# Kernel tuning notes

Hardware: AMD Instinct MI355X
Metric: run time of the kernel (lower is better)

## Reference

```python
import jax, jax.numpy as jnp
import numpy as np

B, T, C = 2, 2048, 2048
H, D, G = 16, 128, 4   # num_heads, head_dim, num_kv_groups
EPS = 1e-6


def setup_inputs() -> dict:
    key = jax.random.key(0)
    ks = jax.random.split(key, 6)
    x = jax.random.normal(ks[0], (B, T, C), dtype=jnp.float32)
    # causal mask: True = disallowed (strictly upper triangular)
    mask = jnp.triu(jnp.ones((T, T), dtype=bool), k=1)
    # RoPE tables, full head_dim with duplicated angle halves
    inv_freq = 1.0 / (10000.0 ** (jnp.arange(0, D, 2, dtype=jnp.float32) / D))
    angles = jnp.arange(T, dtype=jnp.float32)[:, None] * inv_freq[None, :]  # [T, D/2]
    angles = jnp.concatenate([angles, angles], axis=-1)                     # [T, D]
    cos, sin = jnp.cos(angles), jnp.sin(angles)
    std = 0.02
    W_query = jax.random.normal(ks[1], (C, H * D), dtype=jnp.float32) * std
    W_key = jax.random.normal(ks[2], (C, G * D), dtype=jnp.float32) * std
    W_value = jax.random.normal(ks[3], (C, G * D), dtype=jnp.float32) * std
    W_out = jax.random.normal(ks[4], (H * D, C), dtype=jnp.float32) * std
    q_scale = jnp.ones((D,), dtype=jnp.float32)
    k_scale = jnp.ones((D,), dtype=jnp.float32)
    return {"x": x, "mask": mask, "cos": cos, "sin": sin,
            "W_query": W_query, "W_key": W_key, "W_value": W_value,
            "W_out": W_out, "q_scale": q_scale, "k_scale": k_scale}


def _rmsnorm(x, scale):
    # qwen3-compatible: compute in fp32, rescale, cast back
    xf = x.astype(jnp.float32)
    var = jnp.mean(xf * xf, axis=-1, keepdims=True)
    return (xf * jax.lax.rsqrt(var + EPS) * scale).astype(x.dtype)


def _rope(x, cos, sin):
    d = x.shape[-1]
    x1, x2 = x[..., : d // 2], x[..., d // 2 :]
    rotated = jnp.concatenate([-x2, x1], axis=-1)
    # cos/sin: [T, D] -> broadcast over [B, H, T, D]
    return (x * cos[None, None] + rotated * sin[None, None]).astype(x.dtype)


def reference(x, mask, cos, sin, W_query, W_key, W_value, W_out, q_scale, k_scale):
    b, t, _ = x.shape
    Q = (x @ W_query).reshape(b, t, H, D).transpose(0, 2, 1, 3)  # [B,H,T,D]
    K = (x @ W_key).reshape(b, t, G, D).transpose(0, 2, 1, 3)    # [B,G,T,D]
    V = (x @ W_value).reshape(b, t, G, D).transpose(0, 2, 1, 3)
    group_size = H // G
    K = jnp.repeat(K, group_size, axis=1)  # [B,H,T,D]
    V = jnp.repeat(V, group_size, axis=1)
    Q = _rmsnorm(Q, q_scale)
    K = _rmsnorm(K, k_scale)
    Q = _rope(Q, cos, sin)
    K = _rope(K, cos, sin)
    scale = D ** (-0.5)
    attn = jnp.einsum("bhqd,bhkd->bhqk", Q, K) * scale
    attn = jnp.where(mask[None, None], -jnp.inf, attn)
    w = jax.nn.softmax(attn, axis=-1)
    out = jnp.einsum("bhqk,bhkd->bhqd", w, V)
    out = out.transpose(0, 2, 1, 3).reshape(b, t, H * D)
    return out @ W_out
```

## Files before the change

kernel.cpp:

```cpp
#include <hip/hip_runtime.h>
#include <hip/hip_bf16.h>

#define Bq 2
#define Tt 2048
#define Cc 2048
#define Hh 16
#define Dd 128
#define Gg 4

using bf16 = __hip_bfloat16;
typedef __attribute__((ext_vector_type(8))) short short8;
typedef __attribute__((ext_vector_type(4))) float f32x4;

__device__ __forceinline__ void gload_lds16(const void* g, void* l) {
    __builtin_amdgcn_global_load_lds(
        (const __attribute__((address_space(1))) unsigned int*)g,
        (__attribute__((address_space(3))) unsigned int*)l, 16, 0, 0);
}

#define MEMBAR() asm volatile("" ::: "memory")

__global__ void k_cast_bf16(const float* __restrict__ in, bf16* __restrict__ out, int n4) {
    int i = blockIdx.x * blockDim.x + threadIdx.x;
    if (i >= n4) return;
    float4 v = ((const float4*)in)[i];
    union { bf16 h[4]; uint2 u; } u;
    u.h[0] = __float2bfloat16(v.x);
    u.h[1] = __float2bfloat16(v.y);
    u.h[2] = __float2bfloat16(v.z);
    u.h[3] = __float2bfloat16(v.w);
    ((uint2*)out)[i] = u.u;
}

__global__ void k_cast_transpose(const float* __restrict__ in, bf16* __restrict__ out,
                                 int rows, int cols, int ostride) {
    __shared__ float tile[32][33];
    int c0 = blockIdx.x * 32, r0 = blockIdx.y * 32;
    int tx = threadIdx.x, ty = threadIdx.y;
    #pragma unroll
    for (int k = 0; k < 4; ++k)
        tile[ty + 8*k][tx] = in[(size_t)(r0 + ty + 8*k) * cols + c0 + tx];
    __syncthreads();
    #pragma unroll
    for (int k = 0; k < 4; ++k)
        out[(size_t)(c0 + ty + 8*k) * ostride + r0 + tx] = __float2bfloat16(tile[tx][ty + 8*k]);
}

__global__ void k_vt(const bf16* __restrict__ QKV, bf16* __restrict__ Vt) {
    __shared__ bf16 tile[64][65];
    const int d0 = blockIdx.x * 64, t0 = blockIdx.y * 64;
    const int bg = blockIdx.z;
    const int b = bg >> 2, g = bg & 3;
    const int tx = threadIdx.x, ty = threadIdx.y;
    const bf16* src = QKV + (size_t)(b * Tt) * 3072 + 2560 + g * 128;
    #pragma unroll
    for (int k = 0; k < 8; ++k)
        tile[ty + 8*k][tx] = src[(size_t)(t0 + ty + 8*k) * 3072 + d0 + tx];
    __syncthreads();
    bf16* dst = Vt + (size_t)bg * Dd * Tt;
    #pragma unroll
    for (int k = 0; k < 8; ++k)
        dst[(size_t)(d0 + ty + 8*k) * Tt + t0 + tx] = tile[tx][ty + 8*k];
}

template<int OUTF32>
__global__ __launch_bounds__(512, 2)
void k_gemm256(const bf16* __restrict__ A, const bf16* __restrict__ Bt,
               void* __restrict__ C, int M, int N, int K, int nbx) {
    __shared__ __align__(16) bf16 Ls[2][4][128 * 64];
    const int tid = threadIdx.x;
    const int lane = tid & 63;
    const int wid = tid >> 6;
    const int wm = wid >> 2, wn = wid & 3;

    const int nb = gridDim.x;
    const int cpx = nb >> 3;
    const int id = blockIdx.x;
    const int sid = (id & 7) * cpx + (id >> 3);
    const int bx = sid % nbx, by = sid / nbx;
    const int row0 = by * 256, col0 = bx * 256;

    const int NT = K >> 6;
    f32x4 acc[2][4][2][2] = {};

#define STAGE_HT(bufq, tt, ht) {                                               \
        const bool isB_ = ((ht) == 1 || (ht) == 2);                            \
        const int half_ = ((ht) >= 2) ? 128 : 0;                               \
        _Pragma("unroll")                                                      \
        for (int c_ = 0; c_ < 2; ++c_) {                                       \
            const int r_ = c_ * 64 + (tid >> 3);                               \
            const int ch_ = (tid & 7) ^ (r_ & 7);                              \
            const bf16* gs_ = (isB_ ? Bt + (size_t)(col0 + half_ + r_) * K     \
                                    : A  + (size_t)(row0 + half_ + r_) * K)    \
                              + (tt) * 64 + ch_ * 8;                           \
            gload_lds16(gs_, &Ls[bufq][ht][c_ * 4096] + tid * 8);              \
        } }

    STAGE_HT(0, 0, 0); STAGE_HT(0, 0, 1); STAGE_HT(0, 0, 2); STAGE_HT(0, 0, 3);

    for (int t = 0; t < NT; ++t) {
        const int p = t & 1, q = p ^ 1;
        const bool pf = (t + 1 < NT);
        const bf16* hA0 = Ls[p][0];
        const bf16* hB0 = Ls[p][1];
        const bf16* hB1 = Ls[p][2];
        const bf16* hA1 = Ls[p][3];

        short8 af[4][2], bb0[2][2], bb1[2][2];

        auto rdA = [&](const bf16* hh, int i, int kk) -> short8 {
            const int ra = wm * 64 + i * 16 + (lane & 15);
            return *(const short8*)((const char*)hh + ra * 128 +
                   ((kk * 64 + (lane >> 4) * 16) ^ ((ra & 7) << 4)));
        };
        auto rdB = [&](const bf16* hh, int j, int kk) -> short8 {
            const int rb = wn * 32 + j * 16 + (lane & 15);
            return *(const short8*)((const char*)hh + rb * 128 +
                   ((kk * 64 + (lane >> 4) * 16) ^ ((rb & 7) << 4)));
        };

        if (pf) { STAGE_HT(q, t + 1, 0); asm volatile("s_waitcnt vmcnt(6)" ::: "memory"); }
        else    { asm volatile("s_waitcnt vmcnt(4)" ::: "memory"); }
        __builtin_amdgcn_s_barrier(); MEMBAR();
        #pragma unroll
        for (int i = 0; i < 4; ++i)
            #pragma unroll
            for (int kk = 0; kk < 2; ++kk) af[i][kk] = rdA(hA0, i, kk);
        #pragma unroll
        for (int j = 0; j < 2; ++j)
            #pragma unroll
            for (int kk = 0; kk < 2; ++kk) bb0[j][kk] = rdB(hB0, j, kk);
        __builtin_amdgcn_s_setprio(1);
        #pragma unroll
        for (int i = 0; i < 4; ++i)
            #pragma unroll
            for (int j = 0; j < 2; ++j)
                #pragma unroll
                for (int kk = 0; kk < 2; ++kk)
                    acc[0][i][0][j] = __builtin_amdgcn_mfma_f32_16x16x32_bf16(af[i][kk], bb0[j][kk], acc[0][i][0][j], 0, 0, 0);
        __builtin_amdgcn_s_setprio(0);

        MEMBAR();
        if (pf) { STAGE_HT(q, t + 1, 1); asm volatile("s_waitcnt vmcnt(6)" ::: "memory"); }
        else    { asm volatile("s_waitcnt vmcnt(2)" ::: "memory"); }
        __builtin_amdgcn_s_barrier(); MEMBAR();
        #pragma unroll
        for (int j = 0; j < 2; ++j)
            #pragma unroll
            for (int kk = 0; kk < 2; ++kk) bb1[j][kk] = rdB(hB1, j, kk);
        __builtin_amdgcn_s_setprio(1);
        #pragma unroll
        for (int i = 0; i < 4; ++i)
            #pragma unroll
            for (int j = 0; j < 2; ++j)
                #pragma unroll
                for (int kk = 0; kk < 2; ++kk)
                    acc[0][i][1][j] = __builtin_amdgcn_mfma_f32_16x16x32_bf16(af[i][kk], bb1[j][kk], acc[0][i][1][j], 0, 0, 0);
        __builtin_amdgcn_s_setprio(0);

        MEMBAR();
        if (pf) { STAGE_HT(q, t + 1, 2); asm volatile("s_waitcnt vmcnt(6)" ::: "memory"); }
        else    { asm volatile("s_waitcnt vmcnt(0)" ::: "memory"); }
        __builtin_amdgcn_s_barrier(); MEMBAR();
        #pragma unroll
        for (int i = 0; i < 4; ++i)
            #pragma unroll
            for (int kk = 0; kk < 2; ++kk) af[i][kk] = rdA(hA1, i, kk);
        __builtin_amdgcn_s_setprio(1);
        #pragma unroll
        for (int i = 0; i < 4; ++i)
            #pragma unroll
            for (int j = 0; j < 2; ++j)
                #pragma unroll
                for (int kk = 0; kk < 2; ++kk)
                    acc[1][i][1][j] = __builtin_amdgcn_mfma_f32_16x16x32_bf16(af[i][kk], bb1[j][kk], acc[1][i][1][j], 0, 0, 0);
        __builtin_amdgcn_s_setprio(0);

        MEMBAR();
        if (pf) STAGE_HT(q, t + 1, 3);
        __builtin_amdgcn_s_setprio(1);
        #pragma unroll
        for (int i = 0; i < 4; ++i)
            #pragma unroll
            for (int j = 0; j < 2; ++j)
                #pragma unroll
                for (int kk = 0; kk < 2; ++kk)
                    acc[1][i][0][j] = __builtin_amdgcn_mfma_f32_16x16x32_bf16(af[i][kk], bb0[j][kk], acc[1][i][0][j], 0, 0, 0);
        __builtin_amdgcn_s_setprio(0);
        MEMBAR();
        __builtin_amdgcn_s_barrier();
        MEMBAR();
    }
#undef STAGE_HT

    #pragma unroll
    for (int mh = 0; mh < 2; ++mh)
        #pragma unroll
        for (int i = 0; i < 4; ++i)
            #pragma unroll
            for (int nh = 0; nh < 2; ++nh)
                #pragma unroll
                for (int j = 0; j < 2; ++j)
                    #pragma unroll
                    for (int r = 0; r < 4; ++r) {
                        const int crow = row0 + mh * 128 + wm * 64 + i * 16 + (lane >> 4) * 4 + r;
                        const int ccol = col0 + nh * 128 + wn * 32 + j * 16 + (lane & 15);
                        const size_t idx = (size_t)crow * N + ccol;
                        const float v = acc[mh][i][nh][j][r];
                        if (OUTF32) ((float*)C)[idx] = v;
                        else        ((bf16*)C)[idx] = __float2bfloat16(v);
                    }
}

template<int OUTF32>
__global__ __launch_bounds__(256)
void k_gemm_bt(const bf16* __restrict__ A, const bf16* __restrict__ Bt,
               void* __restrict__ C, int M, int N, int K) {
    __shared__ __align__(16) bf16 As[128 * 64];
    __shared__ __align__(16) bf16 Bs[128 * 64];
    const int lane = threadIdx.x & 63;
    const int wave = threadIdx.x >> 6;
    const int row0 = blockIdx.y * 128;
    const int col0 = blockIdx.x * 128;
    const int wm = wave >> 1, wn = wave & 1;
    f32x4 acc[4][4] = {};

    const int srow = lane >> 3;
    const int schunk = ((lane & 7) ^ srow) * 8;

    for (int k0 = 0; k0 < K; k0 += 64) {
        #pragma unroll
        for (int j = 0; j < 4; ++j) {
            const int c = j * 4 + wave;
            const int rt = c * 8 + srow;
            gload_lds16(A  + (size_t)(row0 + rt) * K + k0 + schunk, As + c * 512);
            gload_lds16(Bt + (size_t)(col0 + rt) * K + k0 + schunk, Bs + c * 512);
        }
        __syncthreads();
        #pragma unroll
        for (int kk = 0; kk < 2; ++kk) {
            short8 af[4], bfr[4];
            #pragma unroll
            for (int i = 0; i < 4; ++i) {
                const int ra = wm * 64 + i * 16 + (lane & 15);
                af[i] = *(const short8*)((const char*)As + ra * 128 +
                        ((kk * 64 + (lane >> 4) * 16) ^ ((ra & 7) << 4)));
                const int rb = wn * 64 + i * 16 + (lane & 15);
                bfr[i] = *(const short8*)((const char*)Bs + rb * 128 +
                        ((kk * 64 + (lane >> 4) * 16) ^ ((rb & 7) << 4)));
            }
            __builtin_amdgcn_s_setprio(1);
            #pragma unroll
            for (int i = 0; i < 4; ++i)
                #pragma unroll
                for (int j = 0; j < 4; ++j)
                    acc[i][j] = __builtin_amdgcn_mfma_f32_16x16x32_bf16(af[i], bfr[j], acc[i][j], 0, 0, 0);
            __builtin_amdgcn_s_setprio(0);
        }
        __syncthreads();
    }

    const int crow0 = row0 + wm * 64 + (lane >> 4) * 4;
    const int ccol0 = col0 + wn * 64 + (lane & 15);
    #pragma unroll
    for (int i = 0; i < 4; ++i)
        #pragma unroll
        for (int j = 0; j < 4; ++j)
            #pragma unroll
            for (int r = 0; r < 4; ++r) {
                const size_t idx = (size_t)(crow0 + i * 16 + r) * N + ccol0 + j * 16;
                const float v = acc[i][j][r];
                if (OUTF32) ((float*)C)[idx] = v;
                else        ((bf16*)C)[idx] = __float2bfloat16(v);
            }
}

__global__ void k_qkv_post(const bf16* __restrict__ QKV,
                           const float* __restrict__ cosT, const float* __restrict__ sinT,
                           const float* __restrict__ qs, const float* __restrict__ ks,
                           bf16* __restrict__ Qr, bf16* __restrict__ Kr) {
    const int bt = blockIdx.x;
    const int b = bt >> 11;
    const int t = bt & 2047;
    const int lane = threadIdx.x & 63;
    const int wave = threadIdx.x >> 6;
    const float c1 = cosT[t * 128 + lane],      c2 = cosT[t * 128 + 64 + lane];
    const float s1 = sinT[t * 128 + lane],      s2 = sinT[t * 128 + 64 + lane];
    const float qs1 = qs[lane], qs2 = qs[lane + 64];
    const float ks1 = ks[lane], ks2 = ks[lane + 64];
    const bf16* rowb = QKV + (size_t)bt * 3072;
    for (int rr = wave; rr < 20; rr += 4) {
        const bf16* src = rowb + rr * 128;
        const float x1 = __bfloat162float(src[lane]);
        const float x2 = __bfloat162float(src[lane + 64]);
        bf16* dst;
        if (rr < 16) dst = Qr + ((size_t)(b * Hh + rr) * Tt + t) * 128;
        else         dst = Kr + ((size_t)(b * Gg + (rr - 16)) * Tt + t) * 128;
        float ssum = x1 * x1 + x2 * x2;
        #pragma unroll
        for (int o = 32; o > 0; o >>= 1) ssum += __shfl_xor(ssum, o);
        const float inv = rsqrtf(ssum * (1.0f / 128.0f) + 1e-6f);
        const float post = (rr < 16) ? 0.08838834764831845f : 1.0f;
        const float sc1 = ((rr < 16) ? qs1 : ks1) * inv;
        const float sc2 = ((rr < 16) ? qs2 : ks2) * inv;
        const float y1 = x1 * sc1;
        const float y2 = x2 * sc2;
        dst[lane]      = __float2bfloat16((y1 * c1 - y2 * s1) * post);
        dst[lane + 64] = __float2bfloat16((y2 * c2 + y1 * s2) * post);
    }
}

__global__ __launch_bounds__(256)
void k_attn(const bf16* __restrict__ Qr, const bf16* __restrict__ Kr,
            const bf16* __restrict__ Vt, bf16* __restrict__ AO) {
    __shared__ __align__(16) bf16 Ksm[2][64 * 128];
    __shared__ __align__(16) bf16 Vsm[2][128 * 64];
    __shared__ __align__(16) bf16 Psm[4][16 * 64];
    const int id = blockIdx.x;
    const int bg = id & 7;
    const int wid = id >> 3;
    const int pair = wid & 15;
    const int hg = wid >> 4;
    const int b = bg >> 2, g = bg & 3;
    const int h = g * 4 + hg;
    const int lane = threadIdx.x & 63;
    const int wave = threadIdx.x >> 6;

    const bf16* Kbase = Kr + (size_t)(b * Gg + g) * Tt * Dd;
    const bf16* Vbase = Vt + (size_t)(b * Gg + g) * Dd * Tt;

    for (int pass = 0; pass < 2; ++pass) {
        const int qt = pass ? (31 - pair) : pair;
        const bf16* Qbase = Qr + ((size_t)(b * Hh + h) * Tt + qt * 64) * Dd;

        short8 qf[4];
        #pragma unroll
        for (int kk = 0; kk < 4; ++kk)
            qf[kk] = *(const short8*)(Qbase + (size_t)(wave * 16 + (lane & 15)) * 128 + kk * 32 + (lane >> 4) * 8);

        float l_run[4] = {0.f, 0.f, 0.f, 0.f};
        f32x4 oacc[8];
        #pragma unroll
        for (int j = 0; j < 8; ++j) oacc[j] = (f32x4){0.f, 0.f, 0.f, 0.f};

        {
            #pragma unroll
            for (int j = 0; j < 4; ++j) {
                const int c = j * 4 + wave;
                const int rtk = c * 4 + (lane >> 4);
                const int chk = (lane & 15) ^ (rtk & 7);
                gload_lds16(Kbase + (size_t)rtk * 128 + chk * 8, Ksm[0] + c * 512);
                const int rtv = c * 8 + (lane >> 3);
                const int chv = (lane & 7) ^ ((lane >> 3) & 7);
                gload_lds16(Vbase + (size_t)rtv * Tt + chv * 8, Vsm[0] + c * 512);
            }
        }

        int cur = 0;
        const int nkv = qt + 1;
        for (int tk = 0; tk < nkv; ++tk) {
            __syncthreads();

            if (tk + 1 < nkv) {
                const int k0n = (tk + 1) * 64;
                #pragma unroll
                for (int j = 0; j < 4; ++j) {
                    const int c = j * 4 + wave;
                    const int rtk = c * 4 + (lane >> 4);
                    const int chk = (lane & 15) ^ (rtk & 7);
                    gload_lds16(Kbase + (size_t)(k0n + rtk) * 128 + chk * 8, Ksm[cur ^ 1] + c * 512);
                    const int rtv = c * 8 + (lane >> 3);
                    const int chv = (lane & 7) ^ ((lane >> 3) & 7);
                    gload_lds16(Vbase + (size_t)rtv * Tt + k0n + chv * 8, Vsm[cur ^ 1] + c * 512);
                }
            }

            const bf16* Ks = Ksm[cur];
            const bf16* Vs = Vsm[cur];

            f32x4 s[4];
            #pragma unroll
            for (int nt = 0; nt < 4; ++nt) s[nt] = (f32x4){0.f, 0.f, 0.f, 0.f};
            __builtin_amdgcn_s_setprio(1);
            #pragma unroll
            for (int nt = 0; nt < 4; ++nt) {
                #pragma unroll
                for (int kk = 0; kk < 4; ++kk) {
                    const int rk = nt * 16 + (lane & 15);
                    short8 kf = *(const short8*)((const char*)Ks + rk * 256 +
                                ((kk * 64 + (lane >> 4) * 16) ^ ((rk & 7) << 4)));
                    s[nt] = __builtin_amdgcn_mfma_f32_16x16x32_bf16(qf[kk], kf, s[nt], 0, 0, 0);
                }
            }
            __builtin_amdgcn_s_setprio(0);

            if (tk == nkv - 1) {
                const int qrow = qt * 64 + wave * 16 + (lane >> 4) * 4;
                const int k0 = tk * 64;
                #pragma unroll
                for (int nt = 0; nt < 4; ++nt) {
                    const int kcol = k0 + nt * 16 + (lane & 15);
                    #pragma unroll
                    for (int r = 0; r < 4; ++r)
                        if (kcol > qrow + r) s[nt][r] = -1e30f;
                }
            }

            #pragma unroll
            for (int nt = 0; nt < 4; ++nt)
                #pragma unroll
                for (int r = 0; r < 4; ++r) {
                    const float p = __expf(s[nt][r]);
                    l_run[r] += p;
                    s[nt][r] = p;
                }

            #pragma unroll
            for (int nt = 0; nt < 4; ++nt)
                #pragma unroll
                for (int r = 0; r < 4; ++r) {
                    const int prow = (lane >> 4) * 4 + r;
                    const int pcol = nt * 16 + (lane & 15);
                    *(bf16*)((char*)Psm[wave] + ((prow * 128 + pcol * 2) ^ ((prow & 7) << 4))) =
                        __float2bfloat16(s[nt][r]);
                }
            #pragma unroll
            for (int kk = 0; kk < 2; ++kk) {
                const int pr = lane & 15;
                short8 pf = *(const short8*)((const char*)Psm[wave] + pr * 128 +
                            ((kk * 64 + (lane >> 4) * 16) ^ ((pr & 7) << 4)));
                __builtin_amdgcn_s_setprio(1);
                #pragma unroll
                for (int j = 0; j < 8; ++j) {
                    const int rb = j * 16 + (lane & 15);
                    short8 vf = *(const short8*)((const char*)Vs + rb * 128 +
                                ((kk * 64 + (lane >> 4) * 16) ^ ((rb & 7) << 4)));
                    oacc[j] = __builtin_amdgcn_mfma_f32_16x16x32_bf16(pf, vf, oacc[j], 0, 0, 0);
                }
                __builtin_amdgcn_s_setprio(0);
            }
            cur ^= 1;
        }
        __syncthreads();

        #pragma unroll
        for (int o = 1; o < 16; o <<= 1)
            #pragma unroll
            for (int r = 0; r < 4; ++r) l_run[r] += __shfl_xor(l_run[r], o);

        #pragma unroll
        for (int r = 0; r < 4; ++r) {
            const float inv = 1.0f / l_run[r];
            const int qrow = qt * 64 + wave * 16 + (lane >> 4) * 4 + r;
            bf16* dst = AO + (size_t)(b * Tt + qrow) * 2048 + h * 128 + (lane & 15);
            #pragma unroll
            for (int j = 0; j < 8; ++j)
                dst[j * 16] = __float2bfloat16(oacc[j][r] * inv);
        }
    }
}

extern "C" void kernel_launch(void* const* d_in, const int* in_sizes, int n_in,
                              void* d_out, int out_size, void* d_ws, size_t ws_size,
                              hipStream_t stream) {
    const float* x    = (const float*)d_in[0];
    const float* cosT = (const float*)d_in[2];
    const float* sinT = (const float*)d_in[3];
    const float* Wq   = (const float*)d_in[4];
    const float* Wk   = (const float*)d_in[5];
    const float* Wv   = (const float*)d_in[6];
    const float* Wo   = (const float*)d_in[7];
    const float* qs   = (const float*)d_in[8];
    const float* ks   = (const float*)d_in[9];

    char* ws = (char*)d_ws;
    bf16* xb   = (bf16*)(ws);
    bf16* Wcat = (bf16*)(ws + 16777216);
    bf16* Wot  = (bf16*)(ws + 29360128);
    bf16* QKV  = (bf16*)(ws + 37748736);
    bf16* Qr   = (bf16*)(ws + 62914560);
    bf16* Kr   = (bf16*)(ws + 79691776);
    bf16* Vtp  = (bf16*)(ws + 83886080);
    bf16* AO   = (bf16*)(ws + 88080384);

    k_cast_bf16<<<8192, 256, 0, stream>>>(x, xb, 2097152);
    dim3 tb(32, 8);
    k_cast_transpose<<<dim3(64, 64), tb, 0, stream>>>(Wq, Wcat, 2048, 2048, 2048);
    k_cast_transpose<<<dim3(16, 64), tb, 0, stream>>>(Wk, Wcat + (size_t)2048 * 2048, 2048, 512, 2048);
    k_cast_transpose<<<dim3(16, 64), tb, 0, stream>>>(Wv, Wcat + (size_t)2560 * 2048, 2048, 512, 2048);
    k_cast_transpose<<<dim3(64, 64), tb, 0, stream>>>(Wo, Wot, 2048, 2048, 2048);

    k_gemm256<0><<<192, 512, 0, stream>>>(xb, Wcat, QKV, 4096, 3072, 2048, 12);
    k_qkv_post<<<4096, 256, 0, stream>>>(QKV, cosT, sinT, qs, ks, Qr, Kr);
    k_vt<<<dim3(2, 32, 8), dim3(64, 8), 0, stream>>>(QKV, Vtp);
    k_attn<<<512, 256, 0, stream>>>(Qr, Kr, Vtp, AO);
    k_gemm_bt<1><<<dim3(16, 32), 256, 0, stream>>>(AO, Wot, d_out, 4096, 2048, 2048);
}
```

Before: 199.7 us.

## Split attention KV loop across two blocks by parity and merge partials

New measurement: 224.9 us. +12.6%, slower.

```diff
diff --git a/kernel.cpp b/kernel.cpp
--- a/kernel.cpp
+++ b/kernel.cpp
@@ -311,153 +311,206 @@
 }
 
 __global__ __launch_bounds__(256)
-void k_attn(const bf16* __restrict__ Qr, const bf16* __restrict__ Kr,
-            const bf16* __restrict__ Vt, bf16* __restrict__ AO) {
-    __shared__ __align__(16) bf16 Ksm[2][64 * 128];
-    __shared__ __align__(16) bf16 Vsm[2][128 * 64];
-    __shared__ __align__(16) bf16 Psm[4][16 * 64];
+void k_attn_part(const bf16* __restrict__ Qr, const bf16* __restrict__ Kr,
+                 const bf16* __restrict__ Vt,
+                 bf16* __restrict__ O0, bf16* __restrict__ O1,
+                 float* __restrict__ L0, float* __restrict__ L1) {
+    __shared__ __align__(16) bf16 Ksm[64 * 128];
+    __shared__ __align__(16) bf16 Vsm[128 * 64];
+    __shared__ __align__(16) bf16 Psm[4][32 * 64];
     const int id = blockIdx.x;
     const int bg = id & 7;
-    const int wid = id >> 3;
-    const int pair = wid & 15;
-    const int hg = wid >> 4;
+    const int rr = id >> 3;
+    const int par = rr & 1;
+    const int pairI = (rr >> 1) & 7;
+    const int hg = rr >> 4;
     const int b = bg >> 2, g = bg & 3;
     const int h = g * 4 + hg;
     const int lane = threadIdx.x & 63;
-    const int wave = threadIdx.x >> 6;
+    const int w = threadIdx.x >> 6;
+    const int hi = lane >> 4;
+    const int lq = lane & 15;
+
+    bf16* Op  = par ? O1 : O0;
+    float* Lp = par ? L1 : L0;
 
     const bf16* Kbase = Kr + (size_t)(b * Gg + g) * Tt * Dd;
     const bf16* Vbase = Vt + (size_t)(b * Gg + g) * Dd * Tt;
 
+#define STAGE_KV(k0_) {                                                        \
+        _Pragma("unroll")                                                      \
+        for (int j = 0; j < 4; ++j) {                                          \
+            const int c = j * 4 + w;                                           \
+            const int rtk = c * 4 + (lane >> 4);                               \
+            const int chk = (lane & 15) ^ (rtk & 7);                           \
+            gload_lds16(Kbase + (size_t)((k0_) + rtk) * 128 + chk * 8, Ksm + c * 512); \
+            const int rtv = c * 8 + (lane >> 3);                               \
+            const int chv = (lane & 7) ^ ((lane >> 3) & 7);                    \
+            gload_lds16(Vbase + (size_t)rtv * Tt + (k0_) + chv * 8, Vsm + c * 512);    \
+        } }
+
     for (int pass = 0; pass < 2; ++pass) {
-        const int qt = pass ? (31 - pair) : pair;
-        const bf16* Qbase = Qr + ((size_t)(b * Hh + h) * Tt + qt * 64) * Dd;
-
-        short8 qf[4];
-        #pragma unroll
-        for (int kk = 0; kk < 4; ++kk)
-            qf[kk] = *(const short8*)(Qbase + (size_t)(wave * 16 + (lane & 15)) * 128 + kk * 32 + (lane >> 4) * 8);
-
-        float l_run[4] = {0.f, 0.f, 0.f, 0.f};
-        f32x4 oacc[8];
-        #pragma unroll
-        for (int j = 0; j < 8; ++j) oacc[j] = (f32x4){0.f, 0.f, 0.f, 0.f};
-
-        {
-            #pragma unroll
-            for (int j = 0; j < 4; ++j) {
-                const int c = j * 4 + wave;
-                const int rtk = c * 4 + (lane >> 4);
-                const int chk = (lane & 15) ^ (rtk & 7);
-                gload_lds16(Kbase + (size_t)rtk * 128 + chk * 8, Ksm[0] + c * 512);
-                const int rtv = c * 8 + (lane >> 3);
-                const int chv = (lane & 7) ^ ((lane >> 3) & 7);
-                gload_lds16(Vbase + (size_t)rtv * Tt + chv * 8, Vsm[0] + c * 512);
-            }
-        }
-
-        int cur = 0;
-        const int nkv = qt + 1;
-        for (int tk = 0; tk < nkv; ++tk) {
+        const int qt = pass ? (15 - pairI) : pairI;
+        const int niter = qt + 1;
+        const bf16* Qbase = Qr + ((size_t)(b * Hh + h) * Tt + qt * 128) * Dd;
+
+        short8 qf[2][4];
+        #pragma unroll
+        for (int sub = 0; sub < 2; ++sub)
+            #pragma unroll
+            for (int kk = 0; kk < 4; ++kk)
+                qf[sub][kk] = *(const short8*)(Qbase +
+                    (size_t)(w * 32 + sub * 16 + lq) * 128 + kk * 32 + hi * 8);
+
+        float l_run[2][4] = {};
+        f32x4 oacc[2][8];
+        #pragma unroll
+        for (int sub = 0; sub < 2; ++sub)
+            #pragma unroll
+            for (int j = 0; j < 8; ++j) oacc[sub][j] = (f32x4){0.f, 0.f, 0.f, 0.f};
+
+        STAGE_KV(par * 64);
+
+        for (int i = 0; i < niter; ++i) {
+            const int tk = par + 2 * i;
             __syncthreads();
 
-            if (tk + 1 < nkv) {
-                const int k0n = (tk + 1) * 64;
-                #pragma unroll
-                for (int j = 0; j < 4; ++j) {
-                    const int c = j * 4 + wave;
-                    const int rtk = c * 4 + (lane >> 4);
-                    const int chk = (lane & 15) ^ (rtk & 7);
-                    gload_lds16(Kbase + (size_t)(k0n + rtk) * 128 + chk * 8, Ksm[cur ^ 1] + c * 512);
-                    const int rtv = c * 8 + (lane >> 3);
-                    const int chv = (lane & 7) ^ ((lane >> 3) & 7);
-                    gload_lds16(Vbase + (size_t)rtv * Tt + k0n + chv * 8, Vsm[cur ^ 1] + c * 512);
+            const bf16* Ks = Ksm;
+            const bf16* Vs = Vsm;
+
+            f32x4 s[2][4];
+            #pragma unroll
+            for (int sub = 0; sub < 2; ++sub)
+                #pragma unroll
+                for (int nt = 0; nt < 4; ++nt) s[sub][nt] = (f32x4){0.f, 0.f, 0.f, 0.f};
+            #pragma unroll
+            for (int nt = 0; nt < 4; ++nt) {
+                const int rk = nt * 16 + lq;
+                short8 kf[4];
+                #pragma unroll
+                for (int kk = 0; kk < 4; ++kk)
+                    kf[kk] = *(const short8*)((const char*)Ks + rk * 256 +
+                             ((kk * 64 + hi * 16) ^ ((rk & 7) << 4)));
+                __builtin_amdgcn_s_setprio(1);
+                #pragma unroll
+                for (int sub = 0; sub < 2; ++sub)
+                    #pragma unroll
+                    for (int kk = 0; kk < 4; ++kk)
+                        s[sub][nt] = __builtin_amdgcn_mfma_f32_16x16x32_bf16(qf[sub][kk], kf[kk], s[sub][nt], 0, 0, 0);
+                __builtin_amdgcn_s_setprio(0);
+            }
+
+            if (i == niter - 1) {
+                const int k0 = tk * 64;
+                #pragma unroll
+                for (int sub = 0; sub < 2; ++sub) {
+                    const int qrow = qt * 128 + w * 32 + sub * 16 + hi * 4;
+                    #pragma unroll
+                    for (int nt = 0; nt < 4; ++nt) {
+                        const int kcol = k0 + nt * 16 + lq;
+                        #pragma unroll
+                        for (int r = 0; r < 4; ++r)
+                            if (kcol > qrow + r) s[sub][nt][r] = -1e30f;
+                    }
                 }
             }
 
-            const bf16* Ks = Ksm[cur];
-            const bf16* Vs = Vsm[cur];
-
-            f32x4 s[4];
-            #pragma unroll
-            for (int nt = 0; nt < 4; ++nt) s[nt] = (f32x4){0.f, 0.f, 0.f, 0.f};
-            __builtin_amdgcn_s_setprio(1);
-            #pragma unroll
-            for (int nt = 0; nt < 4; ++nt) {
-                #pragma unroll
-                for (int kk = 0; kk < 4; ++kk) {
-                    const int rk = nt * 16 + (lane & 15);
-                    short8 kf = *(const short8*)((const char*)Ks + rk * 256 +
-                                ((kk * 64 + (lane >> 4) * 16) ^ ((rk & 7) << 4)));
-                    s[nt] = __builtin_amdgcn_mfma_f32_16x16x32_bf16(qf[kk], kf, s[nt], 0, 0, 0);
+            #pragma unroll
+            for (int sub = 0; sub < 2; ++sub)
+                #pragma unroll
+                for (int nt = 0; nt < 4; ++nt)
+                    #pragma unroll
+                    for (int r = 0; r < 4; ++r) {
+                        const float p = __expf(s[sub][nt][r]);
+                        l_run[sub][r] += p;
+                        s[sub][nt][r] = p;
+                    }
+
+            #pragma unroll
+            for (int sub = 0; sub < 2; ++sub)
+                #pragma unroll
+                for (int nt = 0; nt < 4; ++nt)
+                    #pragma unroll
+                    for (int r = 0; r < 4; ++r) {
+                        const int prow = sub * 16 + hi * 4 + r;
+                        const int pcol = nt * 16 + lq;
+                        *(bf16*)((char*)Psm[w] + ((prow * 128 + pcol * 2) ^ ((prow & 7) << 4))) =
+                            __float2bfloat16(s[sub][nt][r]);
+                    }
+
+            #pragma unroll
+            for (int kk = 0; kk < 2; ++kk) {
+                short8 pf[2];
+                #pragma unroll
+                for (int sub = 0; sub < 2; ++sub) {
+                    const int pr = sub * 16 + lq;
+                    pf[sub] = *(const short8*)((const char*)Psm[w] + pr * 128 +
+                              ((kk * 64 + hi * 16) ^ ((pr & 7) << 4)));
                 }
-            }
-            __builtin_amdgcn_s_setprio(0);
-
-            if (tk == nkv - 1) {
-                const int qrow = qt * 64 + wave * 16 + (lane >> 4) * 4;
-                const int k0 = tk * 64;
-                #pragma unroll
-                for (int nt = 0; nt < 4; ++nt) {
-                    const int kcol = k0 + nt * 16 + (lane & 15);
+                __builtin_amdgcn_s_setprio(1);
+                #pragma unroll
+                for (int j = 0; j < 8; ++j) {
+                    const int rb = j * 16 + lq;
+                    short8 vf = *(const short8*)((const char*)Vs + rb * 128 +
+                                ((kk * 64 + hi * 16) ^ ((rb & 7) << 4)));
                     #pragma unroll
-                    for (int r = 0; r < 4; ++r)
-                        if (kcol > qrow + r) s[nt][r] = -1e30f;
-                }
-            }
-
-            #pragma unroll
-            for (int nt = 0; nt < 4; ++nt)
-                #pragma unroll
-                for (int r = 0; r < 4; ++r) {
-                    const float p = __expf(s[nt][r]);
-                    l_run[r] += p;
-                    s[nt][r] = p;
-                }
-
-            #pragma unroll
-            for (int nt = 0; nt < 4; ++nt)
-                #pragma unroll
-                for (int r = 0; r < 4; ++r) {
-                    const int prow = (lane >> 4) * 4 + r;
-                    const int pcol = nt * 16 + (lane & 15);
-                    *(bf16*)((char*)Psm[wave] + ((prow * 128 + pcol * 2) ^ ((prow & 7) << 4))) =
-                        __float2bfloat16(s[nt][r]);
-                }
-            #pragma unroll
-            for (int kk = 0; kk < 2; ++kk) {
-                const int pr = lane & 15;
-                short8 pf = *(const short8*)((const char*)Psm[wave] + pr * 128 +
-                            ((kk * 64 + (lane >> 4) * 16) ^ ((pr & 7) << 4)));
-                __builtin_amdgcn_s_setprio(1);
-                #pragma unroll
-                for (int j = 0; j < 8; ++j) {
-                    const int rb = j * 16 + (lane & 15);
-                    short8 vf = *(const short8*)((const char*)Vs + rb * 128 +
-                                ((kk * 64 + (lane >> 4) * 16) ^ ((rb & 7) << 4)));
-                    oacc[j] = __builtin_amdgcn_mfma_f32_16x16x32_bf16(pf, vf, oacc[j], 0, 0, 0);
+                    for (int sub = 0; sub < 2; ++sub)
+                        oacc[sub][j] = __builtin_amdgcn_mfma_f32_16x16x32_bf16(pf[sub], vf, oacc[sub][j], 0, 0, 0);
                 }
                 __builtin_amdgcn_s_setprio(0);
             }
-            cur ^= 1;
+
+            if (i + 1 < niter) {
+                __syncthreads();
+                STAGE_KV((tk + 2) * 64);
+            }
         }
         __syncthreads();
 
         #pragma unroll
         for (int o = 1; o < 16; o <<= 1)
             #pragma unroll
-            for (int r = 0; r < 4; ++r) l_run[r] += __shfl_xor(l_run[r], o);
-
-        #pragma unroll
-        for (int r = 0; r < 4; ++r) {
-            const float inv = 1.0f / l_run[r];
-            const int qrow = qt * 64 + wave * 16 + (lane >> 4) * 4 + r;
-            bf16* dst = AO + (size_t)(b * Tt + qrow) * 2048 + h * 128 + (lane & 15);
-            #pragma unroll
-            for (int j = 0; j < 8; ++j)
-                dst[j * 16] = __float2bfloat16(oacc[j][r] * inv);
-        }
+            for (int sub = 0; sub < 2; ++sub)
+                #pragma unroll
+                for (int r = 0; r < 4; ++r) l_run[sub][r] += __shfl_xor(l_run[sub][r], o);
+
+        #pragma unroll
+        for (int sub = 0; sub < 2; ++sub)
+            #pragma unroll
+            for (int r = 0; r < 4; ++r) {
+                const int qrow = qt * 128 + w * 32 + sub * 16 + hi * 4 + r;
+                const size_t ridx = (size_t)(b * Hh + h) * Tt + qrow;
+                bf16* dst = Op + ridx * 128 + lq;
+                #pragma unroll
+                for (int j = 0; j < 8; ++j)
+                    dst[j * 16] = __float2bfloat16(oacc[sub][j][r]);
+                if (lq == 0) Lp[ridx] = l_run[sub][r];
+            }
     }
+#undef STAGE_KV
+}
+
+__global__ void k_attn_merge(const bf16* __restrict__ O0, const bf16* __restrict__ O1,
+                             const float* __restrict__ L0, const float* __restrict__ L1,
+                             bf16* __restrict__ AO) {
+    const int bt = blockIdx.x;
+    const int b = bt >> 11, t = bt & 2047;
+    const int e0 = threadIdx.x * 8;
+    const int h = e0 >> 7, d = e0 & 127;
+    const size_t ridx = (size_t)(b * Hh + h) * Tt + t;
+    const size_t idx = ridx * 128 + d;
+    short8 a = *(const short8*)(O0 + idx);
+    short8 c = *(const short8*)(O1 + idx);
+    const float inv = 1.0f / (L0[ridx] + L1[ridx]);
+    short8 o;
+    #pragma unroll
+    for (int k = 0; k < 8; ++k) {
+        union { short s; bf16 v; } ua, uc, uo;
+        ua.s = a[k]; uc.s = c[k];
+        uo.v = __float2bfloat16((__bfloat162float(ua.v) + __bfloat162float(uc.v)) * inv);
+        o[k] = uo.s;
+    }
+    *(short8*)(AO + (size_t)bt * 2048 + e0) = o;
 }
 
 extern "C" void kernel_launch(void* const* d_in, const int* in_sizes, int n_in,
@@ -483,6 +536,11 @@
     bf16* Vtp  = (bf16*)(ws + 83886080);
     bf16* AO   = (bf16*)(ws + 88080384);
 
+    bf16*  O0 = (bf16*)(ws);
+    bf16*  O1 = (bf16*)(ws + 37748736);
+    float* L0 = (float*)(ws + 16777216);
+    float* L1 = (float*)(ws + 16777216 + 524288);
+
     k_cast_bf16<<<8192, 256, 0, stream>>>(x, xb, 2097152);
     dim3 tb(32, 8);
     k_cast_transpose<<<dim3(64, 64), tb, 0, stream>>>(Wq, Wcat, 2048, 2048, 2048);
@@ -493,6 +551,7 @@
     k_gemm256<0><<<192, 512, 0, stream>>>(xb, Wcat, QKV, 4096, 3072, 2048, 12);
     k_qkv_post<<<4096, 256, 0, stream>>>(QKV, cosT, sinT, qs, ks, Qr, Kr);
     k_vt<<<dim3(2, 32, 8), dim3(64, 8), 0, stream>>>(QKV, Vtp);
-    k_attn<<<512, 256, 0, stream>>>(Qr, Kr, Vtp, AO);
+    k_attn_part<<<512, 256, 0, stream>>>(Qr, Kr, Vtp, O0, O1, L0, L1);
+    k_attn_merge<<<4096, 256, 0, stream>>>(O0, O1, L0, L1, AO);
     k_gemm_bt<1><<<dim3(16, 32), 256, 0, stream>>>(AO, Wot, d_out, 4096, 2048, 2048);
 }
```
